# Kernel tuning notes

Hardware: AMD Instinct MI355X
Metric: run time of the kernel (lower is better)

The kernel has to match this reference:

```python
import jax, jax.numpy as jnp
import numpy as np

N, E, G = 100000, 1600000, 5000
F_IN, H = 128, 3
C1, C2, C3 = 64, 32, 16
SLOPE = 0.2


def _gat_conv(x, W, a_src, a_dst, b, src, dst, n_nodes, heads, ch):
    # x: [N, F_in] -> h: [N, H, C]
    h = (x @ W).reshape(n_nodes, heads, ch)
    alpha_s = jnp.sum(h * a_src, axis=-1)  # [N, H]
    alpha_d = jnp.sum(h * a_dst, axis=-1)  # [N, H]
    e = jax.nn.leaky_relu(alpha_s[src] + alpha_d[dst], SLOPE)  # [E, H]
    # segment softmax over destination nodes (numerically stable)
    e_max = jax.ops.segment_max(e, dst, num_segments=n_nodes)
    e_max = jnp.where(jnp.isfinite(e_max), e_max, 0.0)
    ex = jnp.exp(e - e_max[dst])
    denom = jax.ops.segment_sum(ex, dst, num_segments=n_nodes)
    alpha = ex / (denom[dst] + 1e-16)  # [E, H]
    msg = h[src] * alpha[:, :, None]  # [E, H, C]
    out = jax.ops.segment_sum(msg, dst, num_segments=n_nodes)  # [N, H, C]
    return out.reshape(n_nodes, heads * ch) + b


def setup_inputs() -> dict:
    key = jax.random.key(0)
    ks = jax.random.split(key, 20)
    def w(k, shape, fan_in):
        return jax.random.normal(k, shape, jnp.float32) / np.sqrt(fan_in)
    return {
        "x": jax.random.normal(ks[0], (N, F_IN), jnp.float32),
        "y": jax.random.uniform(ks[1], (G,), jnp.float32),
        "edge_index": jax.random.randint(ks[2], (2, E), 0, N, jnp.int32),
        "batch": jnp.sort(jax.random.randint(ks[3], (N,), 0, G, jnp.int32)),
        "W1": w(ks[4], (F_IN, H * C1), F_IN),
        "as1": w(ks[5], (H, C1), C1),
        "ad1": w(ks[6], (H, C1), C1),
        "b1": jnp.zeros((H * C1,), jnp.float32),
        "W2": w(ks[7], (H * C1, H * C2), H * C1),
        "as2": w(ks[8], (H, C2), C2),
        "ad2": w(ks[9], (H, C2), C2),
        "b2": jnp.zeros((H * C2,), jnp.float32),
        "W3": w(ks[10], (H * C2, H * C3), H * C2),
        "as3": w(ks[11], (H, C3), C3),
        "ad3": w(ks[12], (H, C3), C3),
        "b3": jnp.zeros((H * C3,), jnp.float32),
        "Wl": w(ks[13], (H * C3, 1), H * C3),
        "bl": jnp.zeros((1,), jnp.float32),
    }


def reference(x, y, edge_index, batch, W1, as1, ad1, b1, W2, as2, ad2, b2,
              W3, as3, ad3, b3, Wl, bl):
    n = x.shape[0]
    loops = jnp.arange(n, dtype=edge_index.dtype)
    src = jnp.concatenate([edge_index[0], loops])  # PyG add_self_loops=True
    dst = jnp.concatenate([edge_index[1], loops])

    h = _gat_conv(x, W1, as1, ad1, b1, src, dst, n, H, C1)
    h = jax.nn.elu(h)
    h = _gat_conv(h, W2, as2, ad2, b2, src, dst, n, H, C2)
    h = jax.nn.elu(h)
    h = _gat_conv(h, W3, as3, ad3, b3, src, dst, n, H, C3)

    # global mean pool over graphs
    counts = jax.ops.segment_sum(jnp.ones((n,), h.dtype), batch, num_segments=G)
    pooled = jax.ops.segment_sum(h, batch, num_segments=G) / jnp.maximum(counts, 1.0)[:, None]
    pooled = jax.nn.relu(pooled)

    logits = pooled @ Wl + bl  # [G, 1]
    t = y.reshape(-1, 1)
    loss = jnp.mean(jax.nn.softplus(logits) - t * logits)  # BCEWithLogits
    out = jax.nn.sigmoid(logits)
    return out, loss
```

## Files before the change

kernel.cpp:

```cpp
#include <hip/hip_runtime.h>
#include <hip/hip_bf16.h>

#define THREADS 256
typedef __hip_bfloat16 bf16;

typedef __bf16 v8bf __attribute__((ext_vector_type(8)));
typedef float  v4f  __attribute__((ext_vector_type(4)));

__device__ __forceinline__ float bfl(unsigned u){ return __uint_as_float(u << 16); }
__device__ __forceinline__ float bfh(unsigned u){ return __uint_as_float(u & 0xffff0000u); }

__global__ void hist_k(const int* __restrict__ ei, int* __restrict__ cnt,
                       int* __restrict__ rank, int E, int ET){
  int i = blockIdx.x*THREADS + threadIdx.x;
  if (i >= ET) return;
  int d = (i < E) ? ei[E + i] : (i - E);
  rank[i] = atomicAdd(&cnt[d], 1);
}

__global__ void scan1_k(const int* __restrict__ deg, int* __restrict__ off,
                        int* __restrict__ bsum, int n){
  __shared__ int sh[1024];
  int i = blockIdx.x*1024 + threadIdx.x;
  int v = (i < n) ? deg[i] : 0;
  sh[threadIdx.x] = v;
  __syncthreads();
  for (int s = 1; s < 1024; s <<= 1){
    int t = (threadIdx.x >= s) ? sh[threadIdx.x - s] : 0;
    __syncthreads();
    sh[threadIdx.x] += t;
    __syncthreads();
  }
  if (i < n) off[i+1] = sh[threadIdx.x];
  if (threadIdx.x == 1023) bsum[blockIdx.x] = sh[1023];
}

__global__ void scan2_k(int* __restrict__ bsum, int nb){
  __shared__ int sh[256];
  int v = (threadIdx.x < nb) ? bsum[threadIdx.x] : 0;
  sh[threadIdx.x] = v;
  __syncthreads();
  for (int s = 1; s < 256; s <<= 1){
    int t = (threadIdx.x >= s) ? sh[threadIdx.x - s] : 0;
    __syncthreads();
    sh[threadIdx.x] += t;
    __syncthreads();
  }
  if (threadIdx.x < nb) bsum[threadIdx.x] = sh[threadIdx.x] - v;
}

__global__ void scan3_k(int* __restrict__ off, const int* __restrict__ bsum, int n){
  int i = blockIdx.x*1024 + threadIdx.x;
  if (i < n) off[i+1] += bsum[blockIdx.x];
  if (i == 0) off[0] = 0;
}

__global__ void scatter_k(const int* __restrict__ ei, const int* __restrict__ off,
                          const int* __restrict__ rank, int* __restrict__ csr,
                          int E, int ET){
  int i = blockIdx.x*THREADS + threadIdx.x;
  if (i >= ET) return;
  int s, d;
  if (i < E){ s = ei[i]; d = ei[E+i]; } else { s = i - E; d = i - E; }
  csr[off[d] + rank[i]] = s;
}

__device__ __forceinline__ void wt_do(const float* __restrict__ W, bf16* __restrict__ WT,
                                      int K, int COUT, int i){
  int k = i / COUT, c = i - k*COUT;
  WT[(size_t)c*K + k] = __float2bfloat16(W[i]);
}

__device__ __forceinline__ void va_do(const float* __restrict__ W, const float* __restrict__ as,
                                      const float* __restrict__ ad, bf16* __restrict__ WTX,
                                      int K, int C, int COUT, int i){
  int k = i % K, c6 = i / K;
  int h = (c6 < 3) ? c6 : c6 - 3;
  const float* a = ((c6 < 3) ? as : ad) + h*C;
  const float* wp = W + (size_t)k*COUT + h*C;
  float s = 0.f;
  for (int cc = 0; cc < C; cc++) s += wp[cc]*a[cc];
  WTX[(size_t)(COUT + c6)*K + k] = __float2bfloat16(s);
}

__global__ void prep_k(const float* __restrict__ W1, const float* __restrict__ as1, const float* __restrict__ ad1,
                       const float* __restrict__ W2, const float* __restrict__ as2, const float* __restrict__ ad2,
                       const float* __restrict__ W3, const float* __restrict__ as3, const float* __restrict__ ad3,
                       bf16* __restrict__ WT1, bf16* __restrict__ WT2, bf16* __restrict__ WT3,
                       const int* __restrict__ batch, int* __restrict__ goff, int n, int G)
{
  int i = blockIdx.x*THREADS + threadIdx.x;
  if (i < 24576){ wt_do(W1, WT1, 128, 192, i); return; } i -= 24576;
  if (i < 18432){ wt_do(W2, WT2, 192, 96, i); return; }  i -= 18432;
  if (i < 4608) { wt_do(W3, WT3, 96, 48, i); return; }   i -= 4608;
  if (i < 768)  { va_do(W1, as1, ad1, WT1, 128, 64, 192, i); return; } i -= 768;
  if (i < 1152) { va_do(W2, as2, ad2, WT2, 192, 32, 96, i); return; }  i -= 1152;
  if (i < 576)  { va_do(W3, as3, ad3, WT3, 96, 16, 48, i); return; }   i -= 576;
  if (i <= G){
    if (i == G){ goff[G] = n; return; }
    int lo = 0, hi = n;
    while (lo < hi){ int mid = (lo + hi) >> 1; if (batch[mid] < i) lo = mid + 1; else hi = mid; }
    goff[i] = lo;
  }
}

template<int K, int COUT, bool CVT>
__global__ void __launch_bounds__(256) gemm_mfma_k(
    const void* __restrict__ Av, const bf16* __restrict__ BT,
    bf16* __restrict__ C, float* __restrict__ aS4, float* __restrict__ aD4,
    int nRowTiles)
{
  int wave = threadIdx.x >> 6, lane = threadIdx.x & 63;
  int rt = blockIdx.x*4 + wave;
  if (rt >= nRowTiles) return;
  int half = lane & 15;
  int quad = lane >> 4;
  v8bf aF[K/32];
  if constexpr (CVT){
    const float* aBase = (const float*)Av + (size_t)(rt*16 + half)*K + quad*8;
    #pragma unroll
    for (int kk = 0; kk < K/32; kk++){
      float4 f0 = *(const float4*)(aBase + kk*32);
      float4 f1 = *(const float4*)(aBase + kk*32 + 4);
      v8bf t;
      t[0] = (__bf16)f0.x; t[1] = (__bf16)f0.y; t[2] = (__bf16)f0.z; t[3] = (__bf16)f0.w;
      t[4] = (__bf16)f1.x; t[5] = (__bf16)f1.y; t[6] = (__bf16)f1.z; t[7] = (__bf16)f1.w;
      aF[kk] = t;
    }
  } else {
    const __bf16* aBase = (const __bf16*)Av + (size_t)(rt*16 + half)*K + quad*8;
    #pragma unroll
    for (int kk = 0; kk < K/32; kk++) aF[kk] = *(const v8bf*)(aBase + kk*32);
  }
  #pragma unroll
  for (int cb = 0; cb < COUT + 16; cb += 16){
    const __bf16* bBase = (const __bf16*)BT + (size_t)(cb + half)*K + quad*8;
    v4f acc = {0.f, 0.f, 0.f, 0.f};
    #pragma unroll
    for (int kk = 0; kk < K/32; kk++)
      acc = __builtin_amdgcn_mfma_f32_16x16x32_bf16(aF[kk], *(const v8bf*)(bBase + kk*32), acc, 0, 0, 0);
    int orow = rt*16 + quad*4;
    if (cb < COUT){
      bf16* cp = C + (size_t)orow*COUT + cb + half;
      #pragma unroll
      for (int r = 0; r < 4; r++)
        cp[(size_t)r*COUT] = __float2bfloat16(acc[r]);
    } else if (half < 6){
      #pragma unroll
      for (int r = 0; r < 4; r++){
        int row = orow + r;
        if (half < 3) aS4[row*4 + half]     = acc[r];
        else          aD4[row*4 + half - 3] = acc[r];
      }
    }
  }
}

template<int HC, int CSH, int GRP>
__global__ void __launch_bounds__(256) agg_k(
    const int* __restrict__ off, const int* __restrict__ csr,
    const bf16* __restrict__ hbuf,
    const float* __restrict__ aS4, const float* __restrict__ aD4,
    const float* __restrict__ bias,
    float* __restrict__ outF, bf16* __restrict__ outB,
    int n, int doElu)
{
  constexpr int NPW = 64 / GRP;
  constexpr int AL  = HC / 8;
  __shared__ __align__(16) float wls[4][384];
  int tid = threadIdx.x;
  int wave = tid >> 6;
  int lane = tid & 63;
  int q = lane % GRP;
  int grp = lane / GRP;
  int wv = (blockIdx.x*256 + tid) >> 6;
  int node = wv*NPW + grp;
  bool valid = node < n;
  int e0 = 0, e1 = 0;
  float4 ad = {0.f, 0.f, 0.f, 0.f};
  if (valid){
    e0 = off[node]; e1 = off[node+1];
    ad = *(const float4*)(aD4 + 4*node);
  }
  const int hq = (8*q) >> CSH;
  const bool act = valid && (q < AL);
  const unsigned q16 = 16u*q;
  float dh = 0.f;
  float a0 = 0.f, a1 = 0.f, a2 = 0.f, a3 = 0.f;
  float a4 = 0.f, a5 = 0.f, a6 = 0.f, a7 = 0.f;
  float* gbase = &wls[wave][grp*3*GRP*2];
  const float* wh = gbase + hq*GRP*2;
  const char* hb = (const char*)hbuf;

#define ACC8(U,W) \
  a0 += (W)*bfl((U).x); a1 += (W)*bfh((U).x); a2 += (W)*bfl((U).y); a3 += (W)*bfh((U).y); \
  a4 += (W)*bfl((U).z); a5 += (W)*bfh((U).z); a6 += (W)*bfl((U).w); a7 += (W)*bfh((U).w);

  int nch = (e1 - e0 + GRP - 1) / GRP;
  for (int c = 0; c < nch; c++){
    int base = e0 + c*GRP;
    __threadfence_block();
    int j = base + q;
    if (j < e1){
      int s = csr[j];
      float4 av = *(const float4*)(aS4 + 4*s);
      float x0 = av.x + ad.x; x0 = (x0 > 0.f) ? x0 : 0.2f*x0;
      float x1 = av.y + ad.y; x1 = (x1 > 0.f) ? x1 : 0.2f*x1;
      float x2 = av.z + ad.z; x2 = (x2 > 0.f) ? x2 : 0.2f*x2;
      float sf = __int_as_float(s * (HC*2));
      float2 p0 = {__expf(x0), sf};
      float2 p1 = {__expf(x1), sf};
      float2 p2 = {__expf(x2), sf};
      *(float2*)(gbase + (0*GRP + q)*2) = p0;
      *(float2*)(gbase + (1*GRP + q)*2) = p1;
      *(float2*)(gbase + (2*GRP + q)*2) = p2;
    }
    __threadfence_block();
    if (act){
      int lim = e1 - base; if (lim > GRP) lim = GRP;
      int jj = 0;
      for (; jj + 4 <= lim; jj += 4){
        float4 pA = *(const float4*)(wh + jj*2);
        float4 pB = *(const float4*)(wh + jj*2 + 4);
        unsigned o0 = __float_as_uint(pA.y) + q16, o1 = __float_as_uint(pA.w) + q16;
        unsigned o2 = __float_as_uint(pB.y) + q16, o3 = __float_as_uint(pB.w) + q16;
        float w0 = pA.x, w1 = pA.z, w2 = pB.x, w3 = pB.z;
        uint4 u0 = *(const uint4*)(hb + o0);
        uint4 u1 = *(const uint4*)(hb + o1);
        uint4 u2 = *(const uint4*)(hb + o2);
        uint4 u3 = *(const uint4*)(hb + o3);
        dh += w0 + w1 + w2 + w3;
        ACC8(u0, w0);
        ACC8(u1, w1);
        ACC8(u2, w2);
        ACC8(u3, w3);
      }
      for (; jj + 2 <= lim; jj += 2){
        float4 pA = *(const float4*)(wh + jj*2);
        unsigned o0 = __float_as_uint(pA.y) + q16, o1 = __float_as_uint(pA.w) + q16;
        float w0 = pA.x, w1 = pA.z;
        uint4 u0 = *(const uint4*)(hb + o0);
        uint4 u1 = *(const uint4*)(hb + o1);
        dh += w0 + w1;
        ACC8(u0, w0);
        ACC8(u1, w1);
      }
      for (; jj < lim; jj++){
        float2 pw = *(const float2*)(wh + jj*2);
        unsigned o = __float_as_uint(pw.y) + q16;
        float w = pw.x;
        uint4 u = *(const uint4*)(hb + o);
        dh += w;
        ACC8(u, w);
      }
    }
  }
#undef ACC8
  if (act){
    float inv = 1.f / (dh + 1e-16f);
    const float4 bA = *(const float4*)(bias + 8*q);
    const float4 bB = *(const float4*)(bias + 8*q + 4);
    float r0 = a0*inv + bA.x, r1 = a1*inv + bA.y, r2 = a2*inv + bA.z, r3 = a3*inv + bA.w;
    float r4 = a4*inv + bB.x, r5 = a5*inv + bB.y, r6 = a6*inv + bB.z, r7 = a7*inv + bB.w;
    if (doElu){
      r0 = (r0 > 0.f) ? r0 : (__expf(r0) - 1.f);
      r1 = (r1 > 0.f) ? r1 : (__expf(r1) - 1.f);
      r2 = (r2 > 0.f) ? r2 : (__expf(r2) - 1.f);
      r3 = (r3 > 0.f) ? r3 : (__expf(r3) - 1.f);
      r4 = (r4 > 0.f) ? r4 : (__expf(r4) - 1.f);
      r5 = (r5 > 0.f) ? r5 : (__expf(r5) - 1.f);
      r6 = (r6 > 0.f) ? r6 : (__expf(r6) - 1.f);
      r7 = (r7 > 0.f) ? r7 : (__expf(r7) - 1.f);
    }
    if (outF){
      float4 oA = {r0, r1, r2, r3};
      float4 oB = {r4, r5, r6, r7};
      *(float4*)(outF + (size_t)node*HC + 8*q)     = oA;
      *(float4*)(outF + (size_t)node*HC + 8*q + 4) = oB;
    }
    if (outB){
      union { bf16 h[8]; uint4 u; } cv;
      cv.h[0] = __float2bfloat16(r0); cv.h[1] = __float2bfloat16(r1);
      cv.h[2] = __float2bfloat16(r2); cv.h[3] = __float2bfloat16(r3);
      cv.h[4] = __float2bfloat16(r4); cv.h[5] = __float2bfloat16(r5);
      cv.h[6] = __float2bfloat16(r6); cv.h[7] = __float2bfloat16(r7);
      *(uint4*)(outB + (size_t)node*HC + 8*q) = cv.u;
    }
  }
}

__global__ void __launch_bounds__(256) pool_logits_k(
    const float* __restrict__ h3, const int* __restrict__ goff,
    const float* __restrict__ Wl, const float* __restrict__ bl,
    const float* __restrict__ y, float* __restrict__ outp,
    float* __restrict__ lossAcc, int G)
{
  int lane = threadIdx.x & 63;
  int g = (blockIdx.x*256 + threadIdx.x) >> 6;
  if (g >= G) return;
  int n0 = goff[g], n1 = goff[g+1];
  int cnt = n1 - n0;
  float acc = 0.f, acc2 = 0.f, wl = 0.f;
  if (lane < 48){
    wl = Wl[lane];
    const float* p = h3 + (size_t)n0*48 + lane;
    int i = 0;
    for (; i + 2 <= cnt; i += 2){ acc += p[(size_t)i*48]; acc2 += p[(size_t)(i+1)*48]; }
    if (i < cnt) acc += p[(size_t)i*48];
    acc += acc2;
  }
  float inv = 1.f / fmaxf((float)cnt, 1.f);
  float v = fmaxf(acc*inv, 0.f) * wl;
  for (int o = 32; o > 0; o >>= 1) v += __shfl_down(v, o);
  if (lane == 0){
    float logit = v + bl[0];
    outp[g] = 1.f / (1.f + __expf(-logit));
    float t = y[g];
    float sp = (logit > 0.f) ? (logit + log1pf(__expf(-logit))) : log1pf(__expf(logit));
    atomicAdd(lossAcc, sp - t*logit);
  }
}

__global__ void fin_k(const float* __restrict__ lossAcc, float* __restrict__ outp, int gtot){
  outp[gtot] = lossAcc[0] / (float)gtot;
}

extern "C" void kernel_launch(void* const* d_in, const int* in_sizes, int n_in,
                              void* d_out, int out_size, void* d_ws, size_t ws_size,
                              hipStream_t stream)
{
  (void)n_in; (void)out_size; (void)ws_size;
  const float* x    = (const float*)d_in[0];
  const float* y    = (const float*)d_in[1];
  const int*  ei    = (const int*)d_in[2];
  const int*  batch = (const int*)d_in[3];
  const float* W1 = (const float*)d_in[4];
  const float* as1= (const float*)d_in[5];
  const float* ad1= (const float*)d_in[6];
  const float* b1 = (const float*)d_in[7];
  const float* W2 = (const float*)d_in[8];
  const float* as2= (const float*)d_in[9];
  const float* ad2= (const float*)d_in[10];
  const float* b2 = (const float*)d_in[11];
  const float* W3 = (const float*)d_in[12];
  const float* as3= (const float*)d_in[13];
  const float* ad3= (const float*)d_in[14];
  const float* b3 = (const float*)d_in[15];
  const float* Wl = (const float*)d_in[16];
  const float* bl = (const float*)d_in[17];
  float* outp = (float*)d_out;

  int Nn = in_sizes[0] / 128;
  int Gg = in_sizes[1];
  int Ee = in_sizes[2] / 2;
  int ET = Ee + Nn;

  char* p = (char*)d_ws;
  auto carve = [&](size_t bytes) -> void* {
    void* r = (void*)p; p += (bytes + 255) & ~(size_t)255; return r;
  };
  int*   off     = (int*)  carve((size_t)(Nn+1)*4);
  int*   cnt     = (int*)  carve((size_t)Nn*4);
  int*   csr     = (int*)  carve((size_t)ET*4);
  int*   rank    = (int*)  carve((size_t)ET*4);
  int*   bsum    = (int*)  carve(256*4);
  float* aS4     = (float*)carve((size_t)Nn*4*4);
  float* aD4     = (float*)carve((size_t)Nn*4*4);
  int*   goff    = (int*)  carve((size_t)(Gg+1)*4);
  float* lossAcc = (float*)carve(4);
  bf16*  WT1     = (bf16*) carve((size_t)(192+16)*128*2);
  bf16*  WT2     = (bf16*) carve((size_t)(96+16)*192*2);
  bf16*  WT3     = (bf16*) carve((size_t)(48+16)*96*2);
  bf16*  bufH    = (bf16*) carve((size_t)Nn*192*2);
  bf16*  bufA    = (bf16*) carve((size_t)Nn*192*2);
  float* bufO    = (float*)((char*)bufH + ((size_t)Nn*96 + 255 & ~(size_t)255));

  int NB = (Nn + 1023) / 1024;
  int ebk = (ET + THREADS - 1) / THREADS;

  hipMemsetAsync(cnt, 0, (size_t)Nn*4, stream);
  hist_k<<<ebk, THREADS, 0, stream>>>(ei, cnt, rank, Ee, ET);
  scan1_k<<<NB, 1024, 0, stream>>>(cnt, off, bsum, Nn);
  scan2_k<<<1, 256, 0, stream>>>(bsum, NB);
  scan3_k<<<NB, 1024, 0, stream>>>(off, bsum, Nn);
  scatter_k<<<ebk, THREADS, 0, stream>>>(ei, off, rank, csr, Ee, ET);

  int prepTot = 24576 + 18432 + 4608 + 768 + 1152 + 576 + (Gg + 1);
  prep_k<<<(prepTot + THREADS-1)/THREADS, THREADS, 0, stream>>>(
      W1, as1, ad1, W2, as2, ad2, W3, as3, ad3, WT1, WT2, WT3, batch, goff, Nn, Gg);

  int nRT = Nn / 16;
  int gx  = (nRT + 3) / 4;
  int gb1 = (Nn + 3) / 4;
  int gb2 = (Nn + 7) / 8;
  int gb3 = (Nn + 15) / 16;

  gemm_mfma_k<128,192,true><<<gx, 256, 0, stream>>>(x, WT1, bufH, aS4, aD4, nRT);
  agg_k<192,6,64><<<gb1, 256, 0, stream>>>(off, csr, bufH, aS4, aD4, b1, nullptr, bufA, Nn, 1);
  gemm_mfma_k<192,96,false><<<gx, 256, 0, stream>>>(bufA, WT2, bufH, aS4, aD4, nRT);
  agg_k<96,5,32><<<gb2, 256, 0, stream>>>(off, csr, bufH, aS4, aD4, b2, nullptr, bufA, Nn, 1);
  gemm_mfma_k<96,48,false><<<gx, 256, 0, stream>>>(bufA, WT3, bufH, aS4, aD4, nRT);
  agg_k<48,4,16><<<gb3, 256, 0, stream>>>(off, csr, bufH, aS4, aD4, b3, bufO, nullptr, Nn, 0);

  hipMemsetAsync(lossAcc, 0, 4, stream);
  pool_logits_k<<<(Gg + 3)/4, 256, 0, stream>>>(bufO, goff, Wl, bl, y, outp, lossAcc, Gg);
  fin_k<<<1, 1, 0, stream>>>(lossAcc, outp, Gg);
}
```

Measured before the change: 615.3 us.

## Split GAT aggregation into channel slices with edge-parallel lanes and shuffle reduction

The aggregation kernel now assigns one wave per destination node and channel slice, with 8 slices per node spread across blocks. Within a wave, 16 edges are processed in parallel by 4-lane groups, and partial sums are combined with xor-shuffle reductions. The aim is more memory-level parallelism on the gather of neighbour features, replacing the old pattern where few lanes walked edges sequentially. The cost is that attention weights (csr, aS4 loads and exp) are recomputed by all 8 slices, a quarter of lanes sit idle, there is reduction overhead, and gathers in the smaller layers are narrow.

```diff
diff --git a/kernel.cpp b/kernel.cpp
--- a/kernel.cpp
+++ b/kernel.cpp
@@ -156,7 +156,7 @@
   }
 }
 
-template<int HC, int CSH, int GRP>
+template<int HC, int CPL>
 __global__ void __launch_bounds__(256) agg_k(
     const int* __restrict__ off, const int* __restrict__ csr,
     const bf16* __restrict__ hbuf,
@@ -165,126 +165,95 @@
     float* __restrict__ outF, bf16* __restrict__ outB,
     int n, int doElu)
 {
-  constexpr int NPW = 64 / GRP;
-  constexpr int AL  = HC / 8;
-  __shared__ __align__(16) float wls[4][384];
+  constexpr int HPH = HC/3;
+  constexpr int SCH = 3*CPL;
+  __shared__ __align__(16) float4 wls[4][16];
   int tid = threadIdx.x;
-  int wave = tid >> 6;
-  int lane = tid & 63;
-  int q = lane % GRP;
-  int grp = lane / GRP;
-  int wv = (blockIdx.x*256 + tid) >> 6;
-  int node = wv*NPW + grp;
-  bool valid = node < n;
-  int e0 = 0, e1 = 0;
-  float4 ad = {0.f, 0.f, 0.f, 0.f};
-  if (valid){
-    e0 = off[node]; e1 = off[node+1];
-    ad = *(const float4*)(aD4 + 4*node);
-  }
-  const int hq = (8*q) >> CSH;
-  const bool act = valid && (q < AL);
-  const unsigned q16 = 16u*q;
+  int wave = tid >> 6, lane = tid & 63;
+  int e = lane >> 2, c = lane & 3;
+  int slice = blockIdx.x & 7;
+  int node = (int)(blockIdx.x >> 3)*4 + wave;
+  if (node >= n) return;
+  int e0 = off[node], e1 = off[node+1];
+  int cc = (c < 3) ? c : 0;
+  int ch0 = slice*SCH + cc*CPL;
+  int hq = ch0 / HPH;
+  unsigned addOff = (unsigned)(2*ch0);
+  bool cw = (c < 3);
+  float4 ad = *(const float4*)(aD4 + 4*node);
+  const char* hb = (const char*)hbuf;
+  float acc[CPL];
+  #pragma unroll
+  for (int k = 0; k < CPL; k++) acc[k] = 0.f;
   float dh = 0.f;
-  float a0 = 0.f, a1 = 0.f, a2 = 0.f, a3 = 0.f;
-  float a4 = 0.f, a5 = 0.f, a6 = 0.f, a7 = 0.f;
-  float* gbase = &wls[wave][grp*3*GRP*2];
-  const float* wh = gbase + hq*GRP*2;
-  const char* hb = (const char*)hbuf;
-
-#define ACC8(U,W) \
-  a0 += (W)*bfl((U).x); a1 += (W)*bfh((U).x); a2 += (W)*bfl((U).y); a3 += (W)*bfh((U).y); \
-  a4 += (W)*bfl((U).z); a5 += (W)*bfh((U).z); a6 += (W)*bfl((U).w); a7 += (W)*bfh((U).w);
-
-  int nch = (e1 - e0 + GRP - 1) / GRP;
-  for (int c = 0; c < nch; c++){
-    int base = e0 + c*GRP;
+
+  int nch = (e1 - e0 + 15) >> 4;
+  for (int chk = 0; chk < nch; chk++){
+    int base = e0 + chk*16;
     __threadfence_block();
-    int j = base + q;
-    if (j < e1){
-      int s = csr[j];
-      float4 av = *(const float4*)(aS4 + 4*s);
-      float x0 = av.x + ad.x; x0 = (x0 > 0.f) ? x0 : 0.2f*x0;
-      float x1 = av.y + ad.y; x1 = (x1 > 0.f) ? x1 : 0.2f*x1;
-      float x2 = av.z + ad.z; x2 = (x2 > 0.f) ? x2 : 0.2f*x2;
-      float sf = __int_as_float(s * (HC*2));
-      float2 p0 = {__expf(x0), sf};
-      float2 p1 = {__expf(x1), sf};
-      float2 p2 = {__expf(x2), sf};
-      *(float2*)(gbase + (0*GRP + q)*2) = p0;
-      *(float2*)(gbase + (1*GRP + q)*2) = p1;
-      *(float2*)(gbase + (2*GRP + q)*2) = p2;
+    if (c == 0){
+      int j = base + e;
+      float4 wv = {0.f, 0.f, 0.f, __int_as_float(0)};
+      if (j < e1){
+        int s = csr[j];
+        float4 av = *(const float4*)(aS4 + 4*s);
+        float x0 = av.x + ad.x; x0 = (x0 > 0.f) ? x0 : 0.2f*x0;
+        float x1 = av.y + ad.y; x1 = (x1 > 0.f) ? x1 : 0.2f*x1;
+        float x2 = av.z + ad.z; x2 = (x2 > 0.f) ? x2 : 0.2f*x2;
+        wv.x = __expf(x0); wv.y = __expf(x1); wv.z = __expf(x2);
+        wv.w = __int_as_float(s * (HC*2));
+      }
+      wls[wave][e] = wv;
     }
     __threadfence_block();
-    if (act){
-      int lim = e1 - base; if (lim > GRP) lim = GRP;
-      int jj = 0;
-      for (; jj + 4 <= lim; jj += 4){
-        float4 pA = *(const float4*)(wh + jj*2);
-        float4 pB = *(const float4*)(wh + jj*2 + 4);
-        unsigned o0 = __float_as_uint(pA.y) + q16, o1 = __float_as_uint(pA.w) + q16;
-        unsigned o2 = __float_as_uint(pB.y) + q16, o3 = __float_as_uint(pB.w) + q16;
-        float w0 = pA.x, w1 = pA.z, w2 = pB.x, w3 = pB.z;
-        uint4 u0 = *(const uint4*)(hb + o0);
-        uint4 u1 = *(const uint4*)(hb + o1);
-        uint4 u2 = *(const uint4*)(hb + o2);
-        uint4 u3 = *(const uint4*)(hb + o3);
-        dh += w0 + w1 + w2 + w3;
-        ACC8(u0, w0);
-        ACC8(u1, w1);
-        ACC8(u2, w2);
-        ACC8(u3, w3);
+    float4 wv = wls[wave][e];
+    float w = cw ? ((hq == 0) ? wv.x : ((hq == 1) ? wv.y : wv.z)) : 0.f;
+    unsigned o = __float_as_uint(wv.w) + addOff;
+    dh += w;
+    if constexpr (CPL == 8){
+      uint4 u = *(const uint4*)(hb + o);
+      acc[0] += w*bfl(u.x); acc[1] += w*bfh(u.x);
+      acc[2] += w*bfl(u.y); acc[3] += w*bfh(u.y);
+      acc[4] += w*bfl(u.z); acc[5] += w*bfh(u.z);
+      acc[6] += w*bfl(u.w); acc[7] += w*bfh(u.w);
+    } else if constexpr (CPL == 4){
+      uint2 u = *(const uint2*)(hb + o);
+      acc[0] += w*bfl(u.x); acc[1] += w*bfh(u.x);
+      acc[2] += w*bfl(u.y); acc[3] += w*bfh(u.y);
+    } else {
+      unsigned u = *(const unsigned*)(hb + o);
+      acc[0] += w*bfl(u); acc[1] += w*bfh(u);
+    }
+  }
+  #pragma unroll
+  for (int m = 4; m < 64; m <<= 1){
+    dh += __shfl_xor(dh, m, 64);
+    #pragma unroll
+    for (int k = 0; k < CPL; k++) acc[k] += __shfl_xor(acc[k], m, 64);
+  }
+  if (e == 0 && cw){
+    float inv = 1.f / (dh + 1e-16f);
+    float r[CPL];
+    #pragma unroll
+    for (int k = 0; k < CPL; k++) r[k] = acc[k]*inv + bias[ch0 + k];
+    if (doElu){
+      #pragma unroll
+      for (int k = 0; k < CPL; k++) r[k] = (r[k] > 0.f) ? r[k] : (__expf(r[k]) - 1.f);
+    }
+    if (outF){
+      #pragma unroll
+      for (int k = 0; k < CPL; k += 2){
+        float2 o2 = {r[k], r[k+1]};
+        *(float2*)(outF + (size_t)node*HC + ch0 + k) = o2;
       }
-      for (; jj + 2 <= lim; jj += 2){
-        float4 pA = *(const float4*)(wh + jj*2);
-        unsigned o0 = __float_as_uint(pA.y) + q16, o1 = __float_as_uint(pA.w) + q16;
-        float w0 = pA.x, w1 = pA.z;
-        uint4 u0 = *(const uint4*)(hb + o0);
-        uint4 u1 = *(const uint4*)(hb + o1);
-        dh += w0 + w1;
-        ACC8(u0, w0);
-        ACC8(u1, w1);
-      }
-      for (; jj < lim; jj++){
-        float2 pw = *(const float2*)(wh + jj*2);
-        unsigned o = __float_as_uint(pw.y) + q16;
-        float w = pw.x;
-        uint4 u = *(const uint4*)(hb + o);
-        dh += w;
-        ACC8(u, w);
-      }
-    }
-  }
-#undef ACC8
-  if (act){
-    float inv = 1.f / (dh + 1e-16f);
-    const float4 bA = *(const float4*)(bias + 8*q);
-    const float4 bB = *(const float4*)(bias + 8*q + 4);
-    float r0 = a0*inv + bA.x, r1 = a1*inv + bA.y, r2 = a2*inv + bA.z, r3 = a3*inv + bA.w;
-    float r4 = a4*inv + bB.x, r5 = a5*inv + bB.y, r6 = a6*inv + bB.z, r7 = a7*inv + bB.w;
-    if (doElu){
-      r0 = (r0 > 0.f) ? r0 : (__expf(r0) - 1.f);
-      r1 = (r1 > 0.f) ? r1 : (__expf(r1) - 1.f);
-      r2 = (r2 > 0.f) ? r2 : (__expf(r2) - 1.f);
-      r3 = (r3 > 0.f) ? r3 : (__expf(r3) - 1.f);
-      r4 = (r4 > 0.f) ? r4 : (__expf(r4) - 1.f);
-      r5 = (r5 > 0.f) ? r5 : (__expf(r5) - 1.f);
-      r6 = (r6 > 0.f) ? r6 : (__expf(r6) - 1.f);
-      r7 = (r7 > 0.f) ? r7 : (__expf(r7) - 1.f);
-    }
-    if (outF){
-      float4 oA = {r0, r1, r2, r3};
-      float4 oB = {r4, r5, r6, r7};
-      *(float4*)(outF + (size_t)node*HC + 8*q)     = oA;
-      *(float4*)(outF + (size_t)node*HC + 8*q + 4) = oB;
     }
     if (outB){
-      union { bf16 h[8]; uint4 u; } cv;
-      cv.h[0] = __float2bfloat16(r0); cv.h[1] = __float2bfloat16(r1);
-      cv.h[2] = __float2bfloat16(r2); cv.h[3] = __float2bfloat16(r3);
-      cv.h[4] = __float2bfloat16(r4); cv.h[5] = __float2bfloat16(r5);
-      cv.h[6] = __float2bfloat16(r6); cv.h[7] = __float2bfloat16(r7);
-      *(uint4*)(outB + (size_t)node*HC + 8*q) = cv.u;
+      union { bf16 h[8]; uint4 u4; uint2 u2; unsigned u1; } cv;
+      #pragma unroll
+      for (int k = 0; k < CPL; k++) cv.h[k] = __float2bfloat16(r[k]);
+      if constexpr (CPL == 8)      *(uint4*)(outB + (size_t)node*HC + ch0) = cv.u4;
+      else if constexpr (CPL == 4) *(uint2*)(outB + (size_t)node*HC + ch0) = cv.u2;
+      else                         *(unsigned*)(outB + (size_t)node*HC + ch0) = cv.u1;
     }
   }
 }
@@ -391,16 +360,14 @@
 
   int nRT = Nn / 16;
   int gx  = (nRT + 3) / 4;
-  int gb1 = (Nn + 3) / 4;
-  int gb2 = (Nn + 7) / 8;
-  int gb3 = (Nn + 15) / 16;
+  int gbS = 8 * ((Nn + 3) / 4);
 
   gemm_mfma_k<128,192,true><<<gx, 256, 0, stream>>>(x, WT1, bufH, aS4, aD4, nRT);
-  agg_k<192,6,64><<<gb1, 256, 0, stream>>>(off, csr, bufH, aS4, aD4, b1, nullptr, bufA, Nn, 1);
+  agg_k<192,8><<<gbS, 256, 0, stream>>>(off, csr, bufH, aS4, aD4, b1, nullptr, bufA, Nn, 1);
   gemm_mfma_k<192,96,false><<<gx, 256, 0, stream>>>(bufA, WT2, bufH, aS4, aD4, nRT);
-  agg_k<96,5,32><<<gb2, 256, 0, stream>>>(off, csr, bufH, aS4, aD4, b2, nullptr, bufA, Nn, 1);
+  agg_k<96,4><<<gbS, 256, 0, stream>>>(off, csr, bufH, aS4, aD4, b2, nullptr, bufA, Nn, 1);
   gemm_mfma_k<96,48,false><<<gx, 256, 0, stream>>>(bufA, WT3, bufH, aS4, aD4, nRT);
-  agg_k<48,4,16><<<gb3, 256, 0, stream>>>(off, csr, bufH, aS4, aD4, b3, bufO, nullptr, Nn, 0);
+  agg_k<48,2><<<gbS, 256, 0, stream>>>(off, csr, bufH, aS4, aD4, b3, bufO, nullptr, Nn, 0);
 
   hipMemsetAsync(lossAcc, 0, 4, stream);
   pool_logits_k<<<(Gg + 3)/4, 256, 0, stream>>>(bufO, goff, Wl, bl, y, outp, lossAcc, Gg);
```

After: 1.611 ms. +161.8%, slower.
